# Performance work log

Hardware: AMD Instinct MI355X
Metric: run time of the kernel (lower is better)

Reference implementation:

```python
import jax, jax.numpy as jnp
import numpy as np


def setup_inputs() -> dict:
    key = jax.random.key(0)
    k1, k2 = jax.random.split(key)
    B, C, H, W = 16, 4, 768, 768
    img = jax.random.normal(k1, (B, C, H, W), dtype=jnp.float32)
    # dense displacement field (voxel units), 2 channels for (y, x) with 'ij' indexing
    trf = jax.random.normal(k2, (B, 2, H, W), dtype=jnp.float32)
    return {"img": img, "trf": trf}


def _warp_linear(vol, disp):
    # vol:  [B, H, W, C]   disp: [B, H, W, 2] (ij displacements)
    B, H, W, C = vol.shape
    dt = vol.dtype
    gy, gx = jnp.meshgrid(jnp.arange(H, dtype=dt), jnp.arange(W, dtype=dt), indexing='ij')
    loc = jnp.stack([gy, gx], axis=-1)[None] + disp          # absolute sample locations [B,H,W,2]
    max_loc = jnp.array([H - 1, W - 1], dtype=dt)
    clipped = jnp.clip(loc, 0.0, max_loc)
    loc0 = jnp.clip(jnp.floor(loc), 0.0, max_loc)
    loc1 = jnp.clip(loc0 + 1.0, 0.0, max_loc)
    d1 = loc1 - clipped                                       # weight of the floor corner (neurite convention)
    d0 = 1.0 - d1                                             # weight of the ceil corner
    i0 = loc0.astype(jnp.int32)
    i1 = loc1.astype(jnp.int32)
    vol_flat = vol.reshape(B, H * W, C)

    def gather(iy, ix):
        flat = (iy * W + ix).reshape(B, H * W)
        return jnp.take_along_axis(vol_flat, flat[..., None], axis=1).reshape(B, H, W, C)

    corners = [
        (i0[..., 0], d1[..., 0], i0[..., 1], d1[..., 1]),
        (i0[..., 0], d1[..., 0], i1[..., 1], d0[..., 1]),
        (i1[..., 0], d0[..., 0], i0[..., 1], d1[..., 1]),
        (i1[..., 0], d0[..., 0], i1[..., 1], d0[..., 1]),
    ]
    out = jnp.zeros_like(vol)
    for iy, wy, ix, wx in corners:
        out = out + (wy * wx)[..., None] * gather(iy, ix)
    return out


def reference(img, trf):
    # faithful to SpatialTransformer.forward with a dense 2D warp, 'ij' indexing,
    # linear interpolation, fill_value=None (edge clamping), single_transform=False
    vol = jnp.transpose(img, (0, 2, 3, 1))   # [B,H,W,C]
    disp = jnp.transpose(trf, (0, 2, 3, 1))  # [B,H,W,2]
    out = _warp_linear(vol, disp)
    return jnp.transpose(out, (0, 3, 1, 2))  # back to [B,C,H,W]
```

## Files before the change

kernel.cpp:

```cpp
#include <hip/hip_runtime.h>


#define BB 16
#define CC 4
#define HH 768
#define WW 768
#define HWSZ (HH * WW)

__global__ __launch_bounds__(256) void st_warp_kernel(
    const float* __restrict__ img,
    const float* __restrict__ trf,
    float* __restrict__ out)
{
    int idx = blockIdx.x * blockDim.x + threadIdx.x;
    if (idx >= BB * HWSZ) return;

    int b = idx / HWSZ;
    int p = idx - b * HWSZ;
    int h = p / WW;
    int w = p - h * WW;

    const float* tb = trf + (size_t)b * 2 * HWSZ;
    float dy = tb[p];
    float dx = tb[p + HWSZ];

    float y = (float)h + dy;
    float x = (float)w + dx;

    const float maxy = (float)(HH - 1);
    const float maxx = (float)(WW - 1);

    float cy = fminf(fmaxf(y, 0.0f), maxy);
    float cx = fminf(fmaxf(x, 0.0f), maxx);

    float f0y = fminf(fmaxf(floorf(y), 0.0f), maxy);
    float f0x = fminf(fmaxf(floorf(x), 0.0f), maxx);
    float f1y = fminf(f0y + 1.0f, maxy);
    float f1x = fminf(f0x + 1.0f, maxx);

    float wy0 = f1y - cy;
    float wx0 = f1x - cx;
    float wy1 = 1.0f - wy0;
    float wx1 = 1.0f - wx0;

    int i0y = (int)f0y;
    int i0x = (int)f0x;
    int i1y = (int)f1y;
    int i1x = (int)f1x;

    int o00 = i0y * WW + i0x;
    int o01 = i0y * WW + i1x;
    int o10 = i1y * WW + i0x;
    int o11 = i1y * WW + i1x;

    float w00 = wy0 * wx0;
    float w01 = wy0 * wx1;
    float w10 = wy1 * wx0;
    float w11 = wy1 * wx1;

    const float* ib = img + (size_t)b * CC * HWSZ;
    float* ob = out + (size_t)b * CC * HWSZ + p;

#pragma unroll
    for (int c = 0; c < CC; ++c) {
        const float* ic = ib + c * HWSZ;
        float v = w00 * ic[o00] + w01 * ic[o01] + w10 * ic[o10] + w11 * ic[o11];
        ob[c * HWSZ] = v;
    }
}

extern "C" void kernel_launch(void* const* d_in, const int* in_sizes, int n_in,
                              void* d_out, int out_size, void* d_ws, size_t ws_size,
                              hipStream_t stream) {
    const float* img = (const float*)d_in[0];
    const float* trf = (const float*)d_in[1];
    float* out = (float*)d_out;

    int npix = BB * HWSZ;
    int block = 256;
    int grid = (npix + block - 1) / block;
    st_warp_kernel<<<grid, block, 0, stream>>>(img, trf, out);
}
```

Measured before the change: 381.7 us.

## Tile warp into 2D blocks with XCD-aware tile mapping and nontemporal streams

Each block now covers a 64x16 pixel tile, with every thread processing 4 rows. Blocks are remapped so that consecutive tiles land on the same XCD, which keeps the L2 locality of the gathered image neighbourhoods. Displacement loads and output stores use nontemporal hints so these streams do not evict reused image data from cache. This gives up the simple 1D mapping in exchange for better gather cache reuse; each thread also does more work, which may reduce the memory parallelism available.

```diff
diff --git a/kernel.cpp b/kernel.cpp
--- a/kernel.cpp
+++ b/kernel.cpp
@@ -7,65 +7,86 @@
 #define WW 768
 #define HWSZ (HH * WW)
 
+#define TW 64
+#define TH 16
+#define RPT 4
+#define NXT (WW / TW)
+#define NYT (HH / TH)
+#define TILES_PER_B (NXT * NYT)
+#define NTILES (TILES_PER_B * BB)
+#define NXCD 8
+
 __global__ __launch_bounds__(256) void st_warp_kernel(
     const float* __restrict__ img,
     const float* __restrict__ trf,
     float* __restrict__ out)
 {
-    int idx = blockIdx.x * blockDim.x + threadIdx.x;
-    if (idx >= BB * HWSZ) return;
+    int l = blockIdx.x;
+    int xcd = l & (NXCD - 1);
+    int t = xcd * (NTILES / NXCD) + (l >> 3);
+    int b = t / TILES_PER_B;
+    int rem = t - b * TILES_PER_B;
+    int wt = rem / NYT;
+    int ht = rem - wt * NYT;
 
-    int b = idx / HWSZ;
-    int p = idx - b * HWSZ;
-    int h = p / WW;
-    int w = p - h * WW;
-
-    const float* tb = trf + (size_t)b * 2 * HWSZ;
-    float dy = tb[p];
-    float dx = tb[p + HWSZ];
-
-    float y = (float)h + dy;
-    float x = (float)w + dx;
+    int tx = threadIdx.x & 63;
+    int ty = threadIdx.x >> 6;
+    int w = wt * TW + tx;
+    int h_base = ht * TH + ty * RPT;
 
     const float maxy = (float)(HH - 1);
     const float maxx = (float)(WW - 1);
 
-    float cy = fminf(fmaxf(y, 0.0f), maxy);
-    float cx = fminf(fmaxf(x, 0.0f), maxx);
-
-    float f0y = fminf(fmaxf(floorf(y), 0.0f), maxy);
-    float f0x = fminf(fmaxf(floorf(x), 0.0f), maxx);
-    float f1y = fminf(f0y + 1.0f, maxy);
-    float f1x = fminf(f0x + 1.0f, maxx);
-
-    float wy0 = f1y - cy;
-    float wx0 = f1x - cx;
-    float wy1 = 1.0f - wy0;
-    float wx1 = 1.0f - wx0;
-
-    int i0y = (int)f0y;
-    int i0x = (int)f0x;
-    int i1y = (int)f1y;
-    int i1x = (int)f1x;
-
-    int o00 = i0y * WW + i0x;
-    int o01 = i0y * WW + i1x;
-    int o10 = i1y * WW + i0x;
-    int o11 = i1y * WW + i1x;
-
-    float w00 = wy0 * wx0;
-    float w01 = wy0 * wx1;
-    float w10 = wy1 * wx0;
-    float w11 = wy1 * wx1;
-
+    const float* tb = trf + (size_t)b * 2 * HWSZ;
     const float* ib = img + (size_t)b * CC * HWSZ;
-    float* ob = out + (size_t)b * CC * HWSZ + p;
+    float* ob = out + (size_t)b * CC * HWSZ;
 
 #pragma unroll
-    for (int c = 0; c < CC; ++c) {
-        const float* ic = ib + c * HWSZ;
-        float v = w00 * ic[o00] + w01 * ic[o01] + w10 * ic[o10] + w11 * ic[o11];
-        ob[c * HWSZ] = v;
+    for (int r = 0; r < RPT; ++r) {
+        int h = h_base + r;
+        int p = h * WW + w;
+
+        float dy = __builtin_nontemporal_load(tb + p);
+        float dx = __builtin_nontemporal_load(tb + p + HWSZ);
+
+        float y = (float)h + dy;
+        float x = (float)w + dx;
+
+        float cy = fminf(fmaxf(y, 0.0f), maxy);
+        float cx = fminf(fmaxf(x, 0.0f), maxx);
+
+        float f0y = fminf(fmaxf(floorf(y), 0.0f), maxy);
+        float f0x = fminf(fmaxf(floorf(x), 0.0f), maxx);
+        float f1y = fminf(f0y + 1.0f, maxy);
+        float f1x = fminf(f0x + 1.0f, maxx);
+
+        float wy0 = f1y - cy;
+        float wx0 = f1x - cx;
+        float wy1 = 1.0f - wy0;
+        float wx1 = 1.0f - wx0;
+
+        int i0y = (int)f0y;
+        int i0x = (int)f0x;
+        int i1y = (int)f1y;
+        int i1x = (int)f1x;
+
+        int o00 = i0y * WW + i0x;
+        int o01 = i0y * WW + i1x;
+        int o10 = i1y * WW + i0x;
+        int o11 = i1y * WW + i1x;
+
+        float w00 = wy0 * wx0;
+        float w01 = wy0 * wx1;
+        float w10 = wy1 * wx0;
+        float w11 = wy1 * wx1;
+
+#pragma unroll
+        for (int c = 0; c < CC; ++c) {
+            const float* ic = ib + c * HWSZ;
+            float v = w00 * ic[o00] + w01 * ic[o01]
+                    + w10 * ic[o10] + w11 * ic[o11];
+            __builtin_nontemporal_store(v, ob + c * HWSZ + p);
+        }
     }
 }
 
@@ -76,8 +97,5 @@
     const float* trf = (const float*)d_in[1];
     float* out = (float*)d_out;
 
-    int npix = BB * HWSZ;
-    int block = 256;
-    int grid = (npix + block - 1) / block;
-    st_warp_kernel<<<grid, block, 0, stream>>>(img, trf, out);
+    st_warp_kernel<<<NTILES, 256, 0, stream>>>(img, trf, out);
 }
```

Measured after the change: 365.4 us. -4.3%, faster.
